# Performance work log

Measured on AMD Instinct MI355X. Metric: run time of the kernel, lower is better.

Reference implementation:

```python
import jax, jax.numpy as jnp
import numpy as np


def gcn_conv(h, W, b, src, dst):
    # PyG GCNConv: h @ W, add self-loops, symmetric deg^-1/2 normalization,
    # scatter-add messages from src to dst, then add bias.
    n = h.shape[0]
    h = h @ W                                   # [N, out]
    loop = jnp.arange(n, dtype=src.dtype)
    row = jnp.concatenate([src, loop])          # message sources
    col = jnp.concatenate([dst, loop])          # aggregation targets
    deg = jax.ops.segment_sum(jnp.ones_like(col, dtype=h.dtype), col, num_segments=n)
    dinv = jnp.where(deg > 0, jax.lax.rsqrt(deg), 0.0)
    norm = dinv[row] * dinv[col]                # [E+N]
    out = jax.ops.segment_sum(h[row] * norm[:, None], col, num_segments=n)
    return out + b


def setup_inputs() -> dict:
    key = jax.random.key(0)
    ks = jax.random.split(key, 12)
    N, E = 50000, 800000
    in_dim, hid, out_dim = 768, 256, 128
    x = jax.random.normal(ks[0], (N, in_dim), dtype=jnp.float32)
    edge_index = jax.random.randint(ks[1], (2, E), 0, N, dtype=jnp.int64)

    def lin(k, fan_in, fan_out):
        bound = 1.0 / np.sqrt(fan_in)
        kw, kb = jax.random.split(k)
        W = jax.random.uniform(kw, (fan_in, fan_out), jnp.float32, -bound, bound)
        b = jax.random.uniform(kb, (fan_out,), jnp.float32, -bound, bound)
        return W, b

    W1, b1 = lin(ks[2], in_dim, hid)
    Wg1, bg1 = lin(ks[3], hid, hid)
    Wg2, bg2 = lin(ks[4], hid, hid)
    W2, b2 = lin(ks[5], hid, out_dim)
    Wc, bc = lin(ks[6], out_dim, 2)
    return {
        "x": x, "edge_index": edge_index,
        "W1": W1, "b1": b1, "Wg1": Wg1, "bg1": bg1,
        "Wg2": Wg2, "bg2": bg2, "W2": W2, "b2": b2,
        "Wc": Wc, "bc": bc, "batch_size": 1024,
    }


def reference(x, edge_index, W1, b1, Wg1, bg1, Wg2, bg2, W2, b2, Wc, bc, batch_size):
    src, dst = edge_index[0], edge_index[1]
    h = jax.nn.relu(x @ W1 + b1)                # linear_relu1
    h = gcn_conv(h, Wg1, bg1, src, dst)         # text1
    # dropout is identity in eval mode
    h = gcn_conv(h, Wg2, bg2, src, dst)         # text2
    h = jax.nn.relu(h @ W2 + b2)                # linear_relu2
    logits = h @ Wc + bc                        # classifier
    return logits[:batch_size]
```

## Files before the change

kernel.cpp:

```cpp
#include <hip/hip_runtime.h>
#include <hip/hip_bf16.h>
#include <cstdint>
#include <cstddef>
#include <type_traits>

typedef _Float16 half8 __attribute__((ext_vector_type(8)));
typedef _Float16 half4v __attribute__((ext_vector_type(4)));
typedef float float4v __attribute__((ext_vector_type(4)));


__global__ void k_zero_int(int* __restrict__ p, int n) {
  int i = blockIdx.x * blockDim.x + threadIdx.x;
  if (i < n) p[i] = 0;
}

__global__ void k_count(const int* __restrict__ dst, int* __restrict__ cnt, int E) {
  int e = blockIdx.x * blockDim.x + threadIdx.x;
  if (e < E) atomicAdd(&cnt[dst[e]], 1);
}

__global__ __launch_bounds__(1024) void k_scan_local(const int* __restrict__ cnt,
                                                     int* __restrict__ rowp,
                                                     int* __restrict__ bsum, int n) {
  __shared__ int sm[1024];
  int tid = threadIdx.x;
  int i = blockIdx.x * 1024 + tid;
  int v = (i < n) ? cnt[i] : 0;
  sm[tid] = v;
  __syncthreads();
  for (int off = 1; off < 1024; off <<= 1) {
    int t = (tid >= off) ? sm[tid - off] : 0;
    __syncthreads();
    sm[tid] += t;
    __syncthreads();
  }
  if (i < n) rowp[i] = sm[tid] - v;
  if (tid == 1023) bsum[blockIdx.x] = sm[1023];
}

__global__ __launch_bounds__(1024) void k_scan_sums(int* __restrict__ bsum, int nb) {
  __shared__ int sm[1024];
  int tid = threadIdx.x;
  int v = (tid < nb) ? bsum[tid] : 0;
  sm[tid] = v;
  __syncthreads();
  for (int off = 1; off < 1024; off <<= 1) {
    int t = (tid >= off) ? sm[tid - off] : 0;
    __syncthreads();
    sm[tid] += t;
    __syncthreads();
  }
  if (tid < nb) bsum[tid] = sm[tid] - v;
}

__global__ void k_finalize(int* __restrict__ rowp, const int* __restrict__ bsum,
                           const int* __restrict__ cnt, int* __restrict__ cursor,
                           float* __restrict__ dinv, int n, int E) {
  int i = blockIdx.x * blockDim.x + threadIdx.x;
  if (i < n) {
    int v = rowp[i] + bsum[i >> 10];
    rowp[i] = v;
    cursor[i] = v;
    dinv[i] = rsqrtf((float)(cnt[i] + 1));
  }
  if (i == 0) rowp[n] = E;
}

__global__ void k_fill(const int* __restrict__ src, const int* __restrict__ dst,
                       int* __restrict__ cursor, int* __restrict__ csr_src, int E) {
  int e = blockIdx.x * blockDim.x + threadIdx.x;
  if (e < E) {
    int pos = atomicAdd(&cursor[dst[e]], 1);
    csr_src[pos] = src[e];
  }
}


__global__ void k_w_convert_all(const float* __restrict__ W1, const float* __restrict__ Wg1,
                                const float* __restrict__ Wg2, _Float16* __restrict__ W1t,
                                _Float16* __restrict__ Wg1t, _Float16* __restrict__ Wg2t,
                                int in_dim, int hid) {
  int idx = blockIdx.x * blockDim.x + threadIdx.x;
  int n1 = in_dim * hid;
  int n2 = hid * hid;
  if (idx < n1) {
    int n = idx / in_dim, k = idx - n * in_dim;
    W1t[idx] = (_Float16)W1[(size_t)k * hid + n];
  } else if (idx < n1 + n2) {
    int i2 = idx - n1;
    int n = i2 / hid, k = i2 - n * hid;
    Wg1t[i2] = (_Float16)Wg1[(size_t)k * hid + n];
  } else if (idx < n1 + 2 * n2) {
    int i2 = idx - n1 - n2;
    int n = i2 / hid, k = i2 - n * hid;
    Wg2t[i2] = (_Float16)Wg2[(size_t)k * hid + n];
  }
}


__device__ __forceinline__ void gl_lds16(const void* g, void* l) {
  __builtin_amdgcn_global_load_lds(
      (const __attribute__((address_space(1))) void*)g,
      (__attribute__((address_space(3))) void*)l, 16, 0, 0);
}

template <typename AT, int RELU, int BIAS, int SCALE>
__global__ __launch_bounds__(512) void k_gemm_mfma(const AT* __restrict__ A,
                                                   const _Float16* __restrict__ Bt,
                                                   const float* __restrict__ bias,
                                                   const float* __restrict__ rowscale,
                                                   _Float16* __restrict__ out,
                                                   int M, int N, int K) {
  __shared__ alignas(16) AT Asm[2][256 * 32];
  __shared__ alignas(16) _Float16 Bsm[2][256 * 32];
  constexpr bool AF32 = std::is_same_v<AT, float>;
  constexpr int RA = AF32 ? 4 : 2;
  constexpr int ABUFB = 256 * 32 * (int)sizeof(AT);
  constexpr int BBUFB = 256 * 32 * 2;

  const int tid = threadIdx.x;
  const int wv = tid >> 6;
  const int ln = tid & 63;
  const int quad = ln >> 4;
  const int l15 = ln & 15;
  const int wm = (wv >> 2) * 128;
  const int wn = (wv & 3) * 64;

  const int bm = (int)blockIdx.x * 256;

  const char* aSrcB[RA];
  int aDstOff[RA];
#pragma unroll
  for (int rr = 0; rr < RA; ++rr) {
    int q = rr * 8192 + wv * 1024 + ln * 16;
    int row, colE;
    if constexpr (AF32) {
      int h = q >> 14;
      row = (q >> 6) & 255;
      colE = ((q & 63) >> 2) + (h << 4);
    } else {
      row = q >> 6;
      colE = (q & 63) >> 1;
    }
    int grow = bm + row; if (grow > M - 1) grow = M - 1;
    aSrcB[rr] = (const char*)(A + (size_t)grow * K + colE);
    aDstOff[rr] = rr * 8192 + wv * 1024;
  }
  const char* bSrcB[2];
  int bDstOff[2];
#pragma unroll
  for (int rr = 0; rr < 2; ++rr) {
    int q = rr * 8192 + wv * 1024 + ln * 16;
    int row = q >> 6;
    int colH = (q & 63) >> 1;
    bSrcB[rr] = (const char*)(Bt + (size_t)row * K + colH);
    bDstOff[rr] = rr * 8192 + wv * 1024;
  }

  float4v acc[8][4];
#pragma unroll
  for (int i = 0; i < 8; ++i)
#pragma unroll
    for (int j = 0; j < 4; ++j) acc[i][j] = (float4v){0.f, 0.f, 0.f, 0.f};

  const int nk = K >> 5;

  {
    char* abase = (char*)&Asm[0][0];
    char* bbase = (char*)&Bsm[0][0];
#pragma unroll
    for (int rr = 0; rr < RA; ++rr) gl_lds16(aSrcB[rr], abase + aDstOff[rr]);
#pragma unroll
    for (int rr = 0; rr < 2; ++rr) gl_lds16(bSrcB[rr], bbase + bDstOff[rr]);
  }
  __syncthreads();

  int buf = 0;
  for (int kt = 0; kt < nk; ++kt) {
    if (kt + 1 < nk) {
      const size_t advA = (size_t)(kt + 1) * 32 * sizeof(AT);
      const size_t advB = (size_t)(kt + 1) * 64;
      char* abase = (char*)&Asm[0][0] + (buf ^ 1) * ABUFB;
      char* bbase = (char*)&Bsm[0][0] + (buf ^ 1) * BBUFB;
#pragma unroll
      for (int rr = 0; rr < RA; ++rr) gl_lds16(aSrcB[rr] + advA, abase + aDstOff[rr]);
#pragma unroll
      for (int rr = 0; rr < 2; ++rr) gl_lds16(bSrcB[rr] + advB, bbase + bDstOff[rr]);
    }

    const AT* Ab = &Asm[buf][0];
    const _Float16* Bb = &Bsm[buf][0];
    half8 bf[4];
#pragma unroll
    for (int j = 0; j < 4; ++j)
      bf[j] = *(const half8*)(Bb + (wn + j * 16 + l15) * 32 + quad * 8);
#pragma unroll
    for (int i = 0; i < 8; ++i) {
      int rowa = wm + i * 16 + l15;
      half8 af;
      if constexpr (AF32) {
        const float* ap = Ab + (quad >> 1) * 4096 + rowa * 16 + (quad & 1) * 8;
        float4v f0 = *(const float4v*)ap;
        float4v f1 = *(const float4v*)(ap + 4);
        af[0] = (_Float16)f0[0]; af[1] = (_Float16)f0[1];
        af[2] = (_Float16)f0[2]; af[3] = (_Float16)f0[3];
        af[4] = (_Float16)f1[0]; af[5] = (_Float16)f1[1];
        af[6] = (_Float16)f1[2]; af[7] = (_Float16)f1[3];
      } else {
        af = *(const half8*)(Ab + rowa * 32 + quad * 8);
      }
#pragma unroll
      for (int j = 0; j < 4; ++j)
        acc[i][j] = __builtin_amdgcn_mfma_f32_16x16x32_f16(af, bf[j], acc[i][j], 0, 0, 0);
    }

    __syncthreads();
    buf ^= 1;
  }

#pragma unroll
  for (int j = 0; j < 4; ++j) {
    int c = wn + j * 16 + l15;
    float bv = BIAS ? bias[c] : 0.f;
#pragma unroll
    for (int i = 0; i < 8; ++i) {
      int rbase = bm + wm + i * 16 + quad * 4;
      float4v a = acc[i][j];
#pragma unroll
      for (int reg = 0; reg < 4; ++reg) {
        int r = rbase + reg;
        if (r < M) {
          float v = a[reg] + bv;
          if (RELU) v = fmaxf(v, 0.f);
          if (SCALE) v *= rowscale[r];
          out[(size_t)r * N + c] = (_Float16)v;
        }
      }
    }
  }
}


template <int RELU, int BIAS>
__global__ __launch_bounds__(256) void k_gemm(const float* __restrict__ A,
                                              const float* __restrict__ B,
                                              const float* __restrict__ bias,
                                              float* __restrict__ C,
                                              int M, int N, int K) {
  __shared__ float As[16][68];
  __shared__ float Bs[16][68];
  const int bm = blockIdx.y * 64;
  const int bn = blockIdx.x * 64;
  const int tid = threadIdx.x;
  const int tr = (tid >> 4) << 2;
  const int tc = (tid & 15) << 2;
  const int lm  = tid >> 2;
  const int lk  = (tid & 3) << 2;
  const int lk2 = tid >> 4;
  const int ln  = (tid & 15) << 2;
  const bool arow_ok = (bm + lm) < M;
  const float* Aptr = A + (size_t)(bm + lm) * K + lk;
  const float* Bptr = B + (size_t)lk2 * N + bn + ln;
  float acc[4][4] = {};
  for (int k0 = 0; k0 < K; k0 += 16) {
    float4 a4 = make_float4(0.f, 0.f, 0.f, 0.f);
    if (arow_ok) a4 = *(const float4*)(Aptr + k0);
    float4 b4 = *(const float4*)(Bptr + (size_t)k0 * N);
    As[lk + 0][lm] = a4.x;
    As[lk + 1][lm] = a4.y;
    As[lk + 2][lm] = a4.z;
    As[lk + 3][lm] = a4.w;
    *(float4*)&Bs[lk2][ln] = b4;
    __syncthreads();
#pragma unroll
    for (int k = 0; k < 16; ++k) {
      float4 av = *(const float4*)&As[k][tr];
      float4 bv = *(const float4*)&Bs[k][tc];
      float a[4] = {av.x, av.y, av.z, av.w};
      float b[4] = {bv.x, bv.y, bv.z, bv.w};
#pragma unroll
      for (int i = 0; i < 4; ++i)
#pragma unroll
        for (int j = 0; j < 4; ++j) acc[i][j] += a[i] * b[j];
    }
    __syncthreads();
  }
  float bias_v[4] = {0.f, 0.f, 0.f, 0.f};
  if (BIAS) {
    float4 bb = *(const float4*)(bias + bn + tc);
    bias_v[0] = bb.x; bias_v[1] = bb.y; bias_v[2] = bb.z; bias_v[3] = bb.w;
  }
#pragma unroll
  for (int i = 0; i < 4; ++i) {
    int r = bm + tr + i;
    if (r < M) {
      float4 o;
      o.x = acc[i][0] + bias_v[0];
      o.y = acc[i][1] + bias_v[1];
      o.z = acc[i][2] + bias_v[2];
      o.w = acc[i][3] + bias_v[3];
      if (RELU) {
        o.x = fmaxf(o.x, 0.f); o.y = fmaxf(o.y, 0.f);
        o.z = fmaxf(o.z, 0.f); o.w = fmaxf(o.w, 0.f);
      }
      *(float4*)&C[(size_t)r * N + bn + tc] = o;
    }
  }
}


template <typename OT>
__global__ __launch_bounds__(256) void k_agg(const _Float16* __restrict__ t,
                                             const int* __restrict__ row_ptr,
                                             const int* __restrict__ csr_src,
                                             const float* __restrict__ dinv,
                                             const float* __restrict__ bias,
                                             OT* __restrict__ out, int n_nodes) {
  int w = (int)((blockIdx.x * 256 + threadIdx.x) >> 6);
  int lane = threadIdx.x & 63;
  if (w >= n_nodes) return;
  float di = dinv[w];
  half4v v = *(const half4v*)(t + (size_t)w * 256 + lane * 4);
  float ax = (float)v[0], ay = (float)v[1], az = (float)v[2], aw = (float)v[3];
  int e0 = row_ptr[w], e1 = row_ptr[w + 1];
  int e = e0;
  for (; e + 4 <= e1; e += 4) {
    int s0 = csr_src[e];
    int s1 = csr_src[e + 1];
    int s2 = csr_src[e + 2];
    int s3 = csr_src[e + 3];
    half4v u0 = *(const half4v*)(t + (size_t)s0 * 256 + lane * 4);
    half4v u1 = *(const half4v*)(t + (size_t)s1 * 256 + lane * 4);
    half4v u2 = *(const half4v*)(t + (size_t)s2 * 256 + lane * 4);
    half4v u3 = *(const half4v*)(t + (size_t)s3 * 256 + lane * 4);
    ax += (float)u0[0] + (float)u1[0] + (float)u2[0] + (float)u3[0];
    ay += (float)u0[1] + (float)u1[1] + (float)u2[1] + (float)u3[1];
    az += (float)u0[2] + (float)u1[2] + (float)u2[2] + (float)u3[2];
    aw += (float)u0[3] + (float)u1[3] + (float)u2[3] + (float)u3[3];
  }
  for (; e < e1; ++e) {
    int s = csr_src[e];
    half4v u = *(const half4v*)(t + (size_t)s * 256 + lane * 4);
    ax += (float)u[0]; ay += (float)u[1]; az += (float)u[2]; aw += (float)u[3];
  }
  const float4 b = ((const float4*)bias)[lane];
  if constexpr (std::is_same_v<OT, float>) {
    float4 o;
    o.x = ax * di + b.x; o.y = ay * di + b.y;
    o.z = az * di + b.z; o.w = aw * di + b.w;
    ((float4*)(out + (size_t)w * 256))[lane] = o;
  } else {
    half4v o;
    o[0] = (_Float16)(ax * di + b.x); o[1] = (_Float16)(ay * di + b.y);
    o[2] = (_Float16)(az * di + b.z); o[3] = (_Float16)(aw * di + b.w);
    *(half4v*)(out + (size_t)w * 256 + lane * 4) = o;
  }
}


__global__ __launch_bounds__(256) void k_cls(const float* __restrict__ h,
                                             const float* __restrict__ Wc,
                                             const float* __restrict__ bc,
                                             float* __restrict__ out, int M, int K) {
  __shared__ float w[512];
  for (int i = threadIdx.x; i < 2 * K; i += 256) w[i] = Wc[i];
  __syncthreads();
  int i = blockIdx.x * 256 + threadIdx.x;
  if (i >= M) return;
  float a0 = bc[0], a1 = bc[1];
  const float* hr = h + (size_t)i * K;
  for (int k = 0; k < K; ++k) {
    float a = hr[k];
    a0 += a * w[2 * k];
    a1 += a * w[2 * k + 1];
  }
  out[2 * i] = a0;
  out[2 * i + 1] = a1;
}


extern "C" void kernel_launch(void* const* d_in, const int* in_sizes, int n_in,
                              void* d_out, int out_size, void* d_ws, size_t ws_size,
                              hipStream_t stream) {
  const float* x   = (const float*)d_in[0];
  const int*   ei  = (const int*)d_in[1];
  const float* W1  = (const float*)d_in[2];
  const float* b1  = (const float*)d_in[3];
  const float* Wg1 = (const float*)d_in[4];
  const float* bg1 = (const float*)d_in[5];
  const float* Wg2 = (const float*)d_in[6];
  const float* bg2 = (const float*)d_in[7];
  const float* W2  = (const float*)d_in[8];
  const float* b2  = (const float*)d_in[9];
  const float* Wc  = (const float*)d_in[10];
  const float* bc  = (const float*)d_in[11];
  float* out = (float*)d_out;

  const int hid     = in_sizes[3];
  const int in_dim  = in_sizes[2] / hid;
  const int out_dim = in_sizes[9];
  const int N       = in_sizes[0] / in_dim;
  const int E       = in_sizes[1] / 2;
  const int Batch   = out_size / 2;

  const int* srcI = ei;
  const int* dstI = ei + E;

  char* ws = (char*)d_ws;
  size_t off = 0;
  auto alloc = [&](size_t bytes) -> void* {
    void* p = ws + off;
    off = (off + bytes + 255) & ~(size_t)255;
    return p;
  };
  _Float16* h0h  = (_Float16*)alloc((size_t)N * hid * 2);
  _Float16* t1h  = (_Float16*)alloc((size_t)N * hid * 2);
  _Float16* h1h  = (_Float16*)alloc((size_t)N * hid * 2);
  _Float16* t2h  = (_Float16*)alloc((size_t)N * hid * 2);
  _Float16* W1t  = (_Float16*)alloc((size_t)in_dim * hid * 2);
  _Float16* Wg1t = (_Float16*)alloc((size_t)hid * hid * 2);
  _Float16* Wg2t = (_Float16*)alloc((size_t)hid * hid * 2);
  float* agg2    = (float*)alloc((size_t)Batch * hid * 4);
  float* h3      = (float*)alloc((size_t)Batch * out_dim * 4);
  float* dinv    = (float*)alloc((size_t)N * 4);
  int*   cnt     = (int*)alloc((size_t)N * 4);
  int*   rowp    = (int*)alloc((size_t)(N + 1) * 4);
  int*   bsum    = (int*)alloc((size_t)1024 * 4);
  int*   cursor  = (int*)alloc((size_t)N * 4);
  int*   csrs    = (int*)alloc((size_t)E * 4);
  (void)ws_size; (void)n_in;

  dim3 blk(256);
  const int nb = (N + 1023) / 1024;

  k_zero_int<<<(N + 255) / 256, blk, 0, stream>>>(cnt, N);
  k_count<<<(E + 255) / 256, blk, 0, stream>>>(dstI, cnt, E);
  k_scan_local<<<nb, 1024, 0, stream>>>(cnt, rowp, bsum, N);
  k_scan_sums<<<1, 1024, 0, stream>>>(bsum, nb);
  k_finalize<<<(N + 255) / 256, blk, 0, stream>>>(rowp, bsum, cnt, cursor, dinv, N, E);
  k_fill<<<(E + 255) / 256, blk, 0, stream>>>(srcI, dstI, cursor, csrs, E);

  {
    int total = in_dim * hid + 2 * hid * hid;
    k_w_convert_all<<<(total + 255) / 256, blk, 0, stream>>>(W1, Wg1, Wg2, W1t, Wg1t, Wg2t, in_dim, hid);
  }

  const int ng = (N + 255) / 256;
  dim3 gblk(512);
  k_gemm_mfma<float, 1, 1, 0><<<dim3(ng), gblk, 0, stream>>>(x, W1t, b1, nullptr, h0h, N, hid, in_dim);
  k_gemm_mfma<_Float16, 0, 0, 1><<<dim3(ng), gblk, 0, stream>>>(h0h, Wg1t, nullptr, dinv, t1h, N, hid, hid);
  k_agg<_Float16><<<(N + 3) / 4, blk, 0, stream>>>(t1h, rowp, csrs, dinv, bg1, h1h, N);
  k_gemm_mfma<_Float16, 0, 0, 1><<<dim3(ng), gblk, 0, stream>>>(h1h, Wg2t, nullptr, dinv, t2h, N, hid, hid);
  k_agg<float><<<(Batch + 3) / 4, blk, 0, stream>>>(t2h, rowp, csrs, dinv, bg2, agg2, Batch);
  k_gemm<1, 1><<<dim3(out_dim / 64, (Batch + 63) / 64), blk, 0, stream>>>(agg2, W2, b2, h3, Batch, out_dim, hid);
  k_cls<<<(Batch + 255) / 256, blk, 0, stream>>>(h3, Wc, bc, out, Batch, out_dim);
}
```

Measured before the change: 535.1 us.

## Triple-buffer GEMM LDS tiles with explicit vmcnt waits and one barrier

Moves the MFMA GEMM from double to triple buffering of the A/B LDS tiles, issuing DMA loads two k-tiles ahead. It replaces the per-iteration __syncthreads with a partial s_waitcnt vmcnt wait plus a single s_barrier, so more loads can stay in flight while MFMAs run. This raises LDS use (the f32-A case grows to about 144KB), which could limit occupancy. It also relies on the hand-counted vmcnt values matching the number of gl_lds16 issues per tile.

```diff
diff --git a/kernel.cpp b/kernel.cpp
--- a/kernel.cpp
+++ b/kernel.cpp
@@ -104,6 +104,18 @@
       (__attribute__((address_space(3))) void*)l, 16, 0, 0);
 }
 
+#define VMCNT(n) asm volatile("s_waitcnt vmcnt(" #n ")" ::: "memory")
+
+template <int RA>
+__device__ __forceinline__ void dma_tile(const char* const (&aS)[RA], const int (&aD)[RA],
+                                         const char* const (&bS)[2], const int (&bD)[2],
+                                         char* ab, char* bb, size_t advA, size_t advB) {
+#pragma unroll
+  for (int rr = 0; rr < RA; ++rr) gl_lds16(aS[rr] + advA, ab + aD[rr]);
+#pragma unroll
+  for (int rr = 0; rr < 2; ++rr) gl_lds16(bS[rr] + advB, bb + bD[rr]);
+}
+
 template <typename AT, int RELU, int BIAS, int SCALE>
 __global__ __launch_bounds__(512) void k_gemm_mfma(const AT* __restrict__ A,
                                                    const _Float16* __restrict__ Bt,
@@ -111,8 +123,8 @@
                                                    const float* __restrict__ rowscale,
                                                    _Float16* __restrict__ out,
                                                    int M, int N, int K) {
-  __shared__ alignas(16) AT Asm[2][256 * 32];
-  __shared__ alignas(16) _Float16 Bsm[2][256 * 32];
+  __shared__ alignas(16) AT Asm[3][256 * 32];
+  __shared__ alignas(16) _Float16 Bsm[3][256 * 32];
   constexpr bool AF32 = std::is_same_v<AT, float>;
   constexpr int RA = AF32 ? 4 : 2;
   constexpr int ABUFB = 256 * 32 * (int)sizeof(AT);
@@ -165,31 +177,34 @@
 
   const int nk = K >> 5;
 
-  {
-    char* abase = (char*)&Asm[0][0];
-    char* bbase = (char*)&Bsm[0][0];
-#pragma unroll
-    for (int rr = 0; rr < RA; ++rr) gl_lds16(aSrcB[rr], abase + aDstOff[rr]);
-#pragma unroll
-    for (int rr = 0; rr < 2; ++rr) gl_lds16(bSrcB[rr], bbase + bDstOff[rr]);
-  }
-  __syncthreads();
-
-  int buf = 0;
+  char* const Ab0 = (char*)&Asm[0][0];
+  char* const Bb0 = (char*)&Bsm[0][0];
+
+  dma_tile<RA>(aSrcB, aDstOff, bSrcB, bDstOff, Ab0, Bb0, 0, 0);
+  dma_tile<RA>(aSrcB, aDstOff, bSrcB, bDstOff, Ab0 + ABUFB, Bb0 + BBUFB,
+               (size_t)32 * sizeof(AT), 64);
+
+  int c0 = 0;
   for (int kt = 0; kt < nk; ++kt) {
     if (kt + 1 < nk) {
-      const size_t advA = (size_t)(kt + 1) * 32 * sizeof(AT);
-      const size_t advB = (size_t)(kt + 1) * 64;
-      char* abase = (char*)&Asm[0][0] + (buf ^ 1) * ABUFB;
-      char* bbase = (char*)&Bsm[0][0] + (buf ^ 1) * BBUFB;
-#pragma unroll
-      for (int rr = 0; rr < RA; ++rr) gl_lds16(aSrcB[rr] + advA, abase + aDstOff[rr]);
-#pragma unroll
-      for (int rr = 0; rr < 2; ++rr) gl_lds16(bSrcB[rr] + advB, bbase + bDstOff[rr]);
-    }
-
-    const AT* Ab = &Asm[buf][0];
-    const _Float16* Bb = &Bsm[buf][0];
+      if constexpr (AF32) { VMCNT(6); } else { VMCNT(4); }
+    } else {
+      VMCNT(0);
+    }
+    __builtin_amdgcn_sched_barrier(0);
+    __builtin_amdgcn_s_barrier();
+    __builtin_amdgcn_sched_barrier(0);
+
+    if (kt + 2 < nk) {
+      int c2 = c0 + 2; if (c2 >= 3) c2 -= 3;
+      dma_tile<RA>(aSrcB, aDstOff, bSrcB, bDstOff,
+                   Ab0 + (size_t)c2 * ABUFB, Bb0 + (size_t)c2 * BBUFB,
+                   (size_t)(kt + 2) * 32 * sizeof(AT), (size_t)(kt + 2) * 64);
+      __builtin_amdgcn_sched_barrier(0);
+    }
+
+    const AT* Ab = &Asm[c0][0];
+    const _Float16* Bb = &Bsm[c0][0];
     half8 bf[4];
 #pragma unroll
     for (int j = 0; j < 4; ++j)
@@ -214,8 +229,7 @@
         acc[i][j] = __builtin_amdgcn_mfma_f32_16x16x32_f16(af, bf[j], acc[i][j], 0, 0, 0);
     }
 
-    __syncthreads();
-    buf ^= 1;
+    c0 = (c0 == 2) ? 0 : c0 + 1;
   }
 
 #pragma unroll
```

Result: no change. 535.3 us (+0.0%).
